# Performance work log

Hardware: AMD Instinct MI355X
Metric: run time of the kernel (lower is better)

Reference implementation:

```python
import jax, jax.numpy as jnp
import numpy as np

KERNELS = ("gaussian", "laplacian", "gaussian", "laplacian")
N, M, D, N_PER = 384, 384, 64, 200


def setup_inputs():
    key = jax.random.key(0)
    kx, ky, kb, kp = jax.random.split(key, 4)
    X = jax.random.normal(kx, (N, D), dtype=jnp.float32)
    Y = jax.random.normal(ky, (M, D), dtype=jnp.float32)
    # positive bandwidths of realistic magnitude for d=64 gaussian/laplacian kernels
    bandwidths = jax.random.uniform(kb, (4,), dtype=jnp.float32) * 8.0 + 4.0
    # each row is a random permutation of n+m indices (torch.randperm equivalent)
    perms = jax.vmap(lambda k: jax.random.permutation(k, N + M))(
        jax.random.split(kp, N_PER)).astype(jnp.int32)
    return {"X": X, "Y": Y, "bandwidths": bandwidths, "perms": perms}


def _pairwise_dist(Z):
    # torch.cdist(Z, Z, p=2); eps keeps sqrt grad finite on the zero diagonal
    sq = jnp.sum(Z * Z, axis=1)
    d2 = jnp.maximum(sq[:, None] + sq[None, :] - 2.0 * (Z @ Z.T), 0.0)
    return jnp.sqrt(d2 + 1e-12)


def reference(X, Y, bandwidths, perms):
    n, m = X.shape[0], Y.shape[0]
    Z = jnp.concatenate([X, Y], axis=0)            # [n+m, d]
    dist = _pairwise_dist(Z)                        # [n+m, n+m]
    idx = jnp.arange(min(n, m))
    perm_X, perm_Y = perms[:, :n], perms[:, n:]    # [n_per, n], [n_per, m]
    U, U_b = [], []
    for i, kern in enumerate(KERNELS):
        b = bandwidths[i]
        if kern == "gaussian":
            K = jnp.exp(-(dist * dist) / (b * b))
        else:  # laplacian
            K = jnp.exp(-dist / b)
        # mmd_u's in-place K_XY[diag]=0 mutates the view of K, so zero first
        K = K.at[idx, n + idx].set(0.0)
        K_XX, K_YY, K_XY = K[:n, :n], K[n:, n:], K[:n, n:]
        mmd = ((K_XX.sum() - jnp.trace(K_XX)) / (n * (n - 1))
               + (K_YY.sum() - jnp.trace(K_YY)) / (m * (m - 1))
               - 2.0 * K_XY.sum() / (n * m))
        U.append(mmd)
        # fast_perm: gather permuted blocks, zero diagonals, reduce per permutation
        diagK = jnp.diagonal(K)
        sXX = K[perm_X[:, :, None], perm_X[:, None, :]].sum((1, 2)) - diagK[perm_X].sum(1)
        sYY = K[perm_Y[:, :, None], perm_Y[:, None, :]].sum((1, 2)) - diagK[perm_Y].sum(1)
        sXY = (K[perm_X[:, :, None], perm_Y[:, None, :]].sum((1, 2))
               - K[perm_X[:, idx], perm_Y[:, idx]].sum(1))
        U_b.append(sXX / (n * (n - 1)) + sYY / (m * (m - 1)) - 2.0 * sXY / (n * m))
    U = jnp.stack(U)[:, None]    # [n_b, 1]  == compute_U_stats U.unsqueeze(1)
    U_b = jnp.stack(U_b)         # [n_b, n_per]
    return jnp.concatenate([U, U_b], axis=1)  # [n_b, 1 + n_per]
```

## Files before the change

### kernel.cpp

```cpp
#include <hip/hip_runtime.h>

#define NTOT 768
#define NHALF 384
#define DDIM 64
#define NPER 200
#define PPAD 256
#define NKER 4
#define CHUNK 192
#define NMB 12
#define NKH 2
#define NB_GEMM 384
#define NPART (NMB * NKH)

typedef __attribute__((ext_vector_type(8))) short short8;
typedef __attribute__((ext_vector_type(4))) float floatx4;

constexpr int K0SZ  = NTOT * NTOT;
constexpr int OF_KH = 0;
constexpr int KH_FLOATS = NKER * K0SZ / 2;
constexpr int OF_RS0 = OF_KH + KH_FLOATS;
constexpr int OF_RSX = OF_RS0 + NKER * NTOT;
constexpr int OF_RSY = OF_RSX + NKER * NTOT;
constexpr int OF_C   = OF_RSY + NKER * NTOT;
constexpr int OF_ROWM = OF_C + NKER * NHALF;
constexpr int OF_COLM = OF_ROWM + NKER * NTOT;
constexpr int OF_SCAL = OF_COLM + NKER * NTOT;
constexpr int OF_STT  = OF_SCAL + 16;
constexpr int STT_FLOATS = PPAD * NTOT / 2;
constexpr int OF_Q0P  = OF_STT + STT_FLOATS;

constexpr int SMEMF = CHUNK * 65 + DDIM + 32;

__device__ __forceinline__ unsigned short f2bf(float f) {
    unsigned int u = __float_as_uint(f);
    return (unsigned short)((u + 0x7FFFu + ((u >> 16) & 1u)) >> 16);
}
__device__ __forceinline__ float bf2f(unsigned short h) {
    return __uint_as_float(((unsigned int)h) << 16);
}

__global__ __launch_bounds__(256) void k_s1(const float* __restrict__ X,
                                            const float* __restrict__ Y,
                                            const float* __restrict__ bw,
                                            const int* __restrict__ perms,
                                            float* __restrict__ ws) {
    __shared__ float smem[SMEMF];
    float* zb   = smem;
    float* zaS  = smem + CHUNK * 65;
    float* redw = zaS + DDIM;
    int bid = blockIdx.x, tid = threadIdx.x;
    int wave = tid >> 6, lane = tid & 63;
    unsigned short* STT = (unsigned short*)(ws + OF_STT);
    unsigned short* KH  = (unsigned short*)(ws + OF_KH);

    if (bid < NPER) {
        if (tid < 192) {
            ((uint2*)(STT + bid * NTOT))[tid] = make_uint2(0u, 0u);
            if (bid < PPAD - NPER)
                ((uint2*)(STT + (NPER + bid) * NTOT))[tid] = make_uint2(0u, 0u);
        }
        __syncthreads();
        int v = perms[bid * NTOT + tid];
        STT[bid * NTOT + v] = 0x3F80;
        if (tid < NHALF - 256) {
            int v2 = perms[bid * NTOT + 256 + tid];
            STT[bid * NTOT + v2] = 0x3F80;
        }
        return;
    }

    int a = bid - NPER;
    const float* za = (a < NHALF) ? X + a * DDIM : Y + (a - NHALF) * DDIM;
    if (tid < DDIM) zaS[tid] = za[tid];
    float ib2[NKER], ib1[NKER];
#pragma unroll
    for (int k = 0; k < NKER; ++k) { float b = bw[k]; ib2[k] = 1.f / (b * b); ib1[k] = 1.f / b; }
    __syncthreads();
    float sqa = 0.f;
#pragma unroll
    for (int d = 0; d < DDIM; ++d) sqa = fmaf(zaS[d], zaS[d], sqa);
    float accX[NKER] = {0.f, 0.f, 0.f, 0.f};
    float accY[NKER] = {0.f, 0.f, 0.f, 0.f};

    for (int c0 = 0; c0 < NTOT; c0 += CHUNK) {
        __syncthreads();
        for (int idx = tid; idx < CHUNK * DDIM; idx += 256) {
            int r = idx >> 6, d = idx & 63;
            int gr = c0 + r;
            const float* zr = (gr < NHALF) ? X + gr * DDIM : Y + (gr - NHALF) * DDIM;
            zb[r * 65 + d] = zr[d];
        }
        __syncthreads();
        if (tid < CHUNK) {
            int b = c0 + tid;
            float dot = 0.f, sqb = 0.f;
#pragma unroll
            for (int d = 0; d < DDIM; ++d) {
                float zv = zb[tid * 65 + d];
                dot = fmaf(zaS[d], zv, dot);
                sqb = fmaf(zv, zv, sqb);
            }
            float d2 = (sqa + sqb) - 2.f * dot;
            if (b == a) d2 = 0.f;
            d2 = fmaxf(d2, 0.f);
            float d2e = d2 + 1e-12f;
            float dist = sqrtf(d2e);
#pragma unroll
            for (int k = 0; k < NKER; ++k) {
                float val = ((k & 1) == 0) ? __expf(-d2e * ib2[k]) : __expf(-dist * ib1[k]);
                KH[k * K0SZ + a * NTOT + b] = f2bf(val);
                if (b < NHALF) accX[k] += val; else accY[k] += val;
                if (a < NHALF && b == a + NHALF) ws[OF_C + k * NHALF + a] = val;
            }
        }
    }
    float vals[8];
#pragma unroll
    for (int k = 0; k < NKER; ++k) { vals[k] = accX[k]; vals[4 + k] = accY[k]; }
#pragma unroll
    for (int off = 32; off > 0; off >>= 1)
#pragma unroll
        for (int v = 0; v < 8; ++v) vals[v] += __shfl_down(vals[v], off, 64);
    __syncthreads();
    if (lane == 0)
#pragma unroll
        for (int v = 0; v < 8; ++v) redw[wave * 8 + v] = vals[v];
    __syncthreads();
    if (tid == 0) {
#pragma unroll
        for (int k = 0; k < NKER; ++k) {
            float sx = redw[k] + redw[8 + k] + redw[16 + k] + redw[24 + k];
            float sy = redw[4 + k] + redw[12 + k] + redw[20 + k] + redw[28 + k];
            ws[OF_RS0 + k * NTOT + a] = sx + sy;
            ws[OF_RSX + k * NTOT + a] = sx;
            ws[OF_RSY + k * NTOT + a] = sy;
        }
    }
}

__global__ __launch_bounds__(256) void k_s2(const float* __restrict__ bw,
                                            float* __restrict__ ws, float* __restrict__ out) {
    __shared__ float smem[256];
    int bid = blockIdx.x, tid = threadIdx.x;
    int wave = tid >> 6, lane = tid & 63;

    if (bid < NB_GEMM) {
        int mb = bid % NMB;
        int t  = bid / NMB;
        int nc = t & 3;
        int t2 = t >> 2;
        int k  = t2 & 3;
        int kh = t2 >> 2;
        int m0 = mb * 64 + wave * 16;
        int n0 = nc * 64;
        int row = lane & 15, quad = lane >> 4;
        const unsigned short* KH  = (const unsigned short*)(ws + OF_KH);
        const unsigned short* STT = (const unsigned short*)(ws + OF_STT);
        const unsigned short* aptr = KH + k * K0SZ + (m0 + row) * NTOT + quad * 8;
        floatx4 acc[4][2];
#pragma unroll
        for (int j = 0; j < 4; ++j)
#pragma unroll
            for (int h = 0; h < 2; ++h) acc[j][h] = (floatx4){0.f, 0.f, 0.f, 0.f};
        int kk0 = kh * (NTOT / 2);
        for (int kk = kk0; kk < kk0 + NTOT / 2; kk += 64) {
            short8 a0 = *(const short8*)(aptr + kk);
            short8 a1 = *(const short8*)(aptr + kk + 32);
#pragma unroll
            for (int j = 0; j < 4; ++j) {
                const unsigned short* bp = STT + (n0 + j * 16 + row) * NTOT + quad * 8 + kk;
                short8 b0 = *(const short8*)(bp);
                short8 b1 = *(const short8*)(bp + 32);
                acc[j][0] = __builtin_amdgcn_mfma_f32_16x16x32_bf16(a0, b0, acc[j][0], 0, 0, 0);
                acc[j][1] = __builtin_amdgcn_mfma_f32_16x16x32_bf16(a1, b1, acc[j][1], 0, 0, 0);
            }
        }
        __syncthreads();
#pragma unroll
        for (int j = 0; j < 4; ++j) {
            const unsigned short* sp = STT + (n0 + j * 16 + row) * NTOT + m0 + quad * 4;
            float p = 0.f;
#pragma unroll
            for (int r = 0; r < 4; ++r) p += (acc[j][0][r] + acc[j][1][r]) * bf2f(sp[r]);
            p += __shfl_down(p, 32, 64);
            p += __shfl_down(p, 16, 64);
            if (lane < 16) smem[wave * 64 + j * 16 + lane] = p;
        }
        __syncthreads();
        if (tid < 64) {
            float s = smem[tid] + smem[64 + tid] + smem[128 + tid] + smem[192 + tid];
            ws[OF_Q0P + (k * NPART + kh * NMB + mb) * PPAD + n0 + tid] = s;
        }
        return;
    }

    int k = bid - NB_GEMM;
    float v[5] = {0.f, 0.f, 0.f, 0.f, 0.f};
    for (int a = tid; a < NTOT; a += 256) v[0] += ws[OF_RS0 + k * NTOT + a];
    for (int a = tid; a < NHALF; a += 256) {
        v[1] += ws[OF_C + k * NHALF + a];
        v[2] += ws[OF_RSX + k * NTOT + a];
        v[3] += ws[OF_RSY + k * NTOT + NHALF + a];
        v[4] += ws[OF_RSY + k * NTOT + a];
    }
#pragma unroll
    for (int off = 32; off > 0; off >>= 1)
#pragma unroll
        for (int j = 0; j < 5; ++j) v[j] += __shfl_down(v[j], off, 64);
    __syncthreads();
    if (lane == 0)
#pragma unroll
        for (int j = 0; j < 5; ++j) smem[wave * 8 + j] = v[j];
    __syncthreads();
    if (tid == 0) {
        float tot0 = smem[0] + smem[8] + smem[16] + smem[24];
        float csum = smem[1] + smem[9] + smem[17] + smem[25];
        float sxx  = smem[2] + smem[10] + smem[18] + smem[26];
        float syy  = smem[3] + smem[11] + smem[19] + smem[27];
        float sxy  = smem[4] + smem[12] + smem[20] + smem[28];
        float b = bw[k];
        float dist0 = sqrtf(1e-12f);
        float dk = ((k & 1) == 0) ? expf(-(dist0 * dist0) / (b * b)) : expf(-dist0 / b);
        ws[OF_SCAL + k * 4 + 0] = tot0 - csum;
        ws[OF_SCAL + k * 4 + 1] = dk;
        double U = ((double)sxx - 384.0 * (double)dk) * (1.0 / 147072.0)
                 + ((double)syy - 384.0 * (double)dk) * (1.0 / 147072.0)
                 - 2.0 * ((double)sxy - (double)csum) * (1.0 / 147456.0);
        out[k * 201] = (float)U;
    }
    for (int idx = tid; idx < NTOT; idx += 256) {
        float r0 = ws[OF_RS0 + k * NTOT + idx];
        float cx = (idx < NHALF)  ? ws[OF_C + k * NHALF + idx] : 0.f;
        float cy = (idx >= NHALF) ? ws[OF_C + k * NHALF + idx - NHALF] : 0.f;
        ws[OF_ROWM + k * NTOT + idx] = r0 - cx;
        ws[OF_COLM + k * NTOT + idx] = r0 - cy;
    }
}

__global__ __launch_bounds__(256) void k_s3(const int* __restrict__ perms,
                                            const float* __restrict__ ws,
                                            float* __restrict__ out) {
    __shared__ float smem[128];
    int p = blockIdx.x, tid = threadIdx.x;
    int wave = tid >> 6, lane = tid & 63;
    const unsigned short* STT = (const unsigned short*)(ws + OF_STT);
    const unsigned short* KH  = (const unsigned short*)(ws + OF_KH);
    float v[16] = {0.f};
    for (int i = tid; i < NHALF; i += 256) {
        int a  = perms[p * NTOT + i];
        int bY = perms[p * NTOT + NHALF + i];
        float si  = bf2f(STT[p * NTOT + i]);
        float si2 = bf2f(STT[p * NTOT + NHALF + i]);
#pragma unroll
        for (int k = 0; k < NKER; ++k) {
            v[k * 4 + 0] += ws[OF_ROWM + k * NTOT + a];
            v[k * 4 + 1] += ws[OF_COLM + k * NTOT + a];
            float kv = bf2f(KH[k * K0SZ + a * NTOT + bY]);
            if (a < NHALF && bY == a + NHALF) kv = 0.f;
            v[k * 4 + 2] += kv;
            v[k * 4 + 3] += ws[OF_C + k * NHALF + i] * si * si2;
        }
    }
#pragma unroll
    for (int off = 32; off > 0; off >>= 1)
#pragma unroll
        for (int j = 0; j < 16; ++j) v[j] += __shfl_down(v[j], off, 64);
    __syncthreads();
    if (lane == 0)
#pragma unroll
        for (int j = 0; j < 16; ++j) smem[wave * 16 + j] = v[j];
    __syncthreads();
    if (tid < 16) smem[64 + tid] = smem[tid] + smem[16 + tid] + smem[32 + tid] + smem[48 + tid];
    __syncthreads();
    if (tid < NKER) {
        int k = tid;
        double rs = smem[64 + k * 4 + 0], cs = smem[64 + k * 4 + 1];
        double pair = smem[64 + k * 4 + 2], qc = smem[64 + k * 4 + 3];
        double total_mod = (double)ws[OF_SCAL + k * 4 + 0];
        double dk        = (double)ws[OF_SCAL + k * 4 + 1];
        double q = -qc;
#pragma unroll
        for (int j = 0; j < NPART; ++j) q += (double)ws[OF_Q0P + (k * NPART + j) * PPAD + p];
        double sXX = q - 384.0 * dk;
        double sYY = total_mod - rs - cs + q - 384.0 * dk;
        double sXY = rs - q - pair;
        out[k * 201 + 1 + p] =
            (float)(sXX * (1.0 / 147072.0) + sYY * (1.0 / 147072.0) - 2.0 * sXY * (1.0 / 147456.0));
    }
}

extern "C" void kernel_launch(void* const* d_in, const int* in_sizes, int n_in,
                              void* d_out, int out_size, void* d_ws, size_t ws_size,
                              hipStream_t stream) {
    const float* X     = (const float*)d_in[0];
    const float* Y     = (const float*)d_in[1];
    const float* bw    = (const float*)d_in[2];
    const int*   perms = (const int*)d_in[3];
    float* ws  = (float*)d_ws;
    float* out = (float*)d_out;

    k_s1<<<NPER + NTOT, 256, 0, stream>>>(X, Y, bw, perms, ws);
    k_s2<<<NB_GEMM + NKER, 256, 0, stream>>>(bw, ws, out);
    k_s3<<<NPER, 256, 0, stream>>>(perms, ws, out);
}
```

Baseline: 107.7 us.

## Tile pairwise-distance stage into 64x64 register-blocked tiles with partial row sums

The distance and kernel-matrix stage now uses 64x64 output tiles, with 4x4 register blocking per thread, instead of one block per row. Each tile writes per-tile partial row sums, and the reduction kernel combines them and also computes the row and column masks in the same pass. The aim is to cut redundant global and LDS reads of Z, use vectorized bf16 stores, and raise arithmetic reuse. The cost is a larger partial-sum buffer and an extra 12-way reduction in stage 2.

```diff
diff --git a/kernel.cpp b/kernel.cpp
--- a/kernel.cpp
+++ b/kernel.cpp
@@ -6,11 +6,12 @@
 #define NPER 200
 #define PPAD 256
 #define NKER 4
-#define CHUNK 192
 #define NMB 12
 #define NKH 2
 #define NB_GEMM 384
 #define NPART (NMB * NKH)
+#define NTILE 12
+#define LDSROW 68
 
 typedef __attribute__((ext_vector_type(8))) short short8;
 typedef __attribute__((ext_vector_type(4))) float floatx4;
@@ -18,10 +19,8 @@
 constexpr int K0SZ  = NTOT * NTOT;
 constexpr int OF_KH = 0;
 constexpr int KH_FLOATS = NKER * K0SZ / 2;
-constexpr int OF_RS0 = OF_KH + KH_FLOATS;
-constexpr int OF_RSX = OF_RS0 + NKER * NTOT;
-constexpr int OF_RSY = OF_RSX + NKER * NTOT;
-constexpr int OF_C   = OF_RSY + NKER * NTOT;
+constexpr int OF_P   = OF_KH + KH_FLOATS;
+constexpr int OF_C   = OF_P + NKER * NTILE * NTOT;
 constexpr int OF_ROWM = OF_C + NKER * NHALF;
 constexpr int OF_COLM = OF_ROWM + NKER * NTOT;
 constexpr int OF_SCAL = OF_COLM + NKER * NTOT;
@@ -29,8 +28,6 @@
 constexpr int STT_FLOATS = PPAD * NTOT / 2;
 constexpr int OF_Q0P  = OF_STT + STT_FLOATS;
 
-constexpr int SMEMF = CHUNK * 65 + DDIM + 32;
-
 __device__ __forceinline__ unsigned short f2bf(float f) {
     unsigned int u = __float_as_uint(f);
     return (unsigned short)((u + 0x7FFFu + ((u >> 16) & 1u)) >> 16);
@@ -44,12 +41,10 @@
                                             const float* __restrict__ bw,
                                             const int* __restrict__ perms,
                                             float* __restrict__ ws) {
-    __shared__ float smem[SMEMF];
-    float* zb   = smem;
-    float* zaS  = smem + CHUNK * 65;
-    float* redw = zaS + DDIM;
+    __shared__ float smem[128 * LDSROW + 128];
+    float* zb  = smem;
+    float* nrm = smem + 128 * LDSROW;
     int bid = blockIdx.x, tid = threadIdx.x;
-    int wave = tid >> 6, lane = tid & 63;
     unsigned short* STT = (unsigned short*)(ws + OF_STT);
     unsigned short* KH  = (unsigned short*)(ws + OF_KH);
 
@@ -69,38 +64,73 @@
         return;
     }
 
-    int a = bid - NPER;
-    const float* za = (a < NHALF) ? X + a * DDIM : Y + (a - NHALF) * DDIM;
-    if (tid < DDIM) zaS[tid] = za[tid];
+    int t  = bid - NPER;
+    int at = t / NTILE, bt = t % NTILE;
+    int a0 = at * 64, b0 = bt * 64;
+    int ta = tid >> 4, tb = tid & 15;
+
     float ib2[NKER], ib1[NKER];
 #pragma unroll
     for (int k = 0; k < NKER; ++k) { float b = bw[k]; ib2[k] = 1.f / (b * b); ib1[k] = 1.f / b; }
-    __syncthreads();
-    float sqa = 0.f;
-#pragma unroll
-    for (int d = 0; d < DDIM; ++d) sqa = fmaf(zaS[d], zaS[d], sqa);
-    float accX[NKER] = {0.f, 0.f, 0.f, 0.f};
-    float accY[NKER] = {0.f, 0.f, 0.f, 0.f};
-
-    for (int c0 = 0; c0 < NTOT; c0 += CHUNK) {
-        __syncthreads();
-        for (int idx = tid; idx < CHUNK * DDIM; idx += 256) {
-            int r = idx >> 6, d = idx & 63;
-            int gr = c0 + r;
-            const float* zr = (gr < NHALF) ? X + gr * DDIM : Y + (gr - NHALF) * DDIM;
-            zb[r * 65 + d] = zr[d];
-        }
-        __syncthreads();
-        if (tid < CHUNK) {
-            int b = c0 + tid;
-            float dot = 0.f, sqb = 0.f;
-#pragma unroll
-            for (int d = 0; d < DDIM; ++d) {
-                float zv = zb[tid * 65 + d];
-                dot = fmaf(zaS[d], zv, dot);
-                sqb = fmaf(zv, zv, sqb);
+
+#pragma unroll
+    for (int it = 0; it < 8; ++it) {
+        int idx = it * 256 + tid;
+        int j = idx >> 4, qf = idx & 15;
+        int g = (j < 64) ? a0 + j : b0 + (j - 64);
+        const float* zr = (g < NHALF) ? X + g * DDIM : Y + (g - NHALF) * DDIM;
+        *(float4*)(zb + j * LDSROW + qf * 4) = *(const float4*)(zr + qf * 4);
+    }
+    __syncthreads();
+    if (tid < 128) {
+        float s = 0.f;
+        const float* zr = zb + tid * LDSROW;
+#pragma unroll
+        for (int d = 0; d < DDIM; d += 4) {
+            float4 zv = *(const float4*)(zr + d);
+            s += zv.x * zv.x + zv.y * zv.y + zv.z * zv.z + zv.w * zv.w;
+        }
+        nrm[tid] = s;
+    }
+    __syncthreads();
+
+    float acc[4][4];
+#pragma unroll
+    for (int r = 0; r < 4; ++r)
+#pragma unroll
+        for (int c = 0; c < 4; ++c) acc[r][c] = 0.f;
+#pragma unroll
+    for (int s = 0; s < 16; ++s) {
+        float4 av[4], bv[4];
+#pragma unroll
+        for (int r = 0; r < 4; ++r) av[r] = *(const float4*)(zb + (ta * 4 + r) * LDSROW + s * 4);
+#pragma unroll
+        for (int c = 0; c < 4; ++c) bv[c] = *(const float4*)(zb + (64 + tb * 4 + c) * LDSROW + s * 4);
+#pragma unroll
+        for (int r = 0; r < 4; ++r)
+#pragma unroll
+            for (int c = 0; c < 4; ++c) {
+                acc[r][c] = fmaf(av[r].x, bv[c].x, acc[r][c]);
+                acc[r][c] = fmaf(av[r].y, bv[c].y, acc[r][c]);
+                acc[r][c] = fmaf(av[r].z, bv[c].z, acc[r][c]);
+                acc[r][c] = fmaf(av[r].w, bv[c].w, acc[r][c]);
             }
-            float d2 = (sqa + sqb) - 2.f * dot;
+    }
+
+    float rs[4][NKER];
+#pragma unroll
+    for (int r = 0; r < 4; ++r)
+#pragma unroll
+        for (int k = 0; k < NKER; ++k) rs[r][k] = 0.f;
+
+#pragma unroll
+    for (int r = 0; r < 4; ++r) {
+        int a = a0 + ta * 4 + r;
+        ushort4 us[NKER];
+#pragma unroll
+        for (int c = 0; c < 4; ++c) {
+            int b = b0 + tb * 4 + c;
+            float d2 = (nrm[ta * 4 + r] + nrm[64 + tb * 4 + c]) - 2.f * acc[r][c];
             if (b == a) d2 = 0.f;
             d2 = fmaxf(d2, 0.f);
             float d2e = d2 + 1e-12f;
@@ -108,32 +138,30 @@
 #pragma unroll
             for (int k = 0; k < NKER; ++k) {
                 float val = ((k & 1) == 0) ? __expf(-d2e * ib2[k]) : __expf(-dist * ib1[k]);
-                KH[k * K0SZ + a * NTOT + b] = f2bf(val);
-                if (b < NHALF) accX[k] += val; else accY[k] += val;
-                if (a < NHALF && b == a + NHALF) ws[OF_C + k * NHALF + a] = val;
+                rs[r][k] += val;
+                unsigned short h = f2bf(val);
+                if (c == 0) us[k].x = h; else if (c == 1) us[k].y = h;
+                else if (c == 2) us[k].z = h; else us[k].w = h;
+                if (bt == at + 6 && tb == ta && c == r)
+                    ws[OF_C + k * NHALF + a] = val;
             }
         }
-    }
-    float vals[8];
-#pragma unroll
-    for (int k = 0; k < NKER; ++k) { vals[k] = accX[k]; vals[4 + k] = accY[k]; }
-#pragma unroll
-    for (int off = 32; off > 0; off >>= 1)
-#pragma unroll
-        for (int v = 0; v < 8; ++v) vals[v] += __shfl_down(vals[v], off, 64);
-    __syncthreads();
-    if (lane == 0)
-#pragma unroll
-        for (int v = 0; v < 8; ++v) redw[wave * 8 + v] = vals[v];
-    __syncthreads();
-    if (tid == 0) {
+#pragma unroll
+        for (int k = 0; k < NKER; ++k)
+            *(ushort4*)(KH + k * K0SZ + a * NTOT + b0 + tb * 4) = us[k];
+    }
+
+#pragma unroll
+    for (int off = 8; off > 0; off >>= 1)
+#pragma unroll
+        for (int r = 0; r < 4; ++r)
+#pragma unroll
+            for (int k = 0; k < NKER; ++k) rs[r][k] += __shfl_down(rs[r][k], off, 64);
+    if (tb == 0) {
 #pragma unroll
         for (int k = 0; k < NKER; ++k) {
-            float sx = redw[k] + redw[8 + k] + redw[16 + k] + redw[24 + k];
-            float sy = redw[4 + k] + redw[12 + k] + redw[20 + k] + redw[28 + k];
-            ws[OF_RS0 + k * NTOT + a] = sx + sy;
-            ws[OF_RSX + k * NTOT + a] = sx;
-            ws[OF_RSY + k * NTOT + a] = sy;
+            float4 pv = make_float4(rs[0][k], rs[1][k], rs[2][k], rs[3][k]);
+            *(float4*)(ws + OF_P + (k * NTILE + bt) * NTOT + a0 + ta * 4) = pv;
         }
     }
 }
@@ -195,13 +223,22 @@
     }
 
     int k = bid - NB_GEMM;
+    const float* Pk = ws + OF_P + k * (NTILE * NTOT);
     float v[5] = {0.f, 0.f, 0.f, 0.f, 0.f};
-    for (int a = tid; a < NTOT; a += 256) v[0] += ws[OF_RS0 + k * NTOT + a];
-    for (int a = tid; a < NHALF; a += 256) {
-        v[1] += ws[OF_C + k * NHALF + a];
-        v[2] += ws[OF_RSX + k * NTOT + a];
-        v[3] += ws[OF_RSY + k * NTOT + NHALF + a];
-        v[4] += ws[OF_RSY + k * NTOT + a];
+    for (int a = tid; a < NTOT; a += 256) {
+        float rsx = 0.f, rsy = 0.f;
+#pragma unroll
+        for (int j = 0; j < 6; ++j)  rsx += Pk[j * NTOT + a];
+#pragma unroll
+        for (int j = 6; j < 12; ++j) rsy += Pk[j * NTOT + a];
+        float rs0 = rsx + rsy;
+        float cx = (a < NHALF)  ? ws[OF_C + k * NHALF + a] : 0.f;
+        float cy = (a >= NHALF) ? ws[OF_C + k * NHALF + a - NHALF] : 0.f;
+        ws[OF_ROWM + k * NTOT + a] = rs0 - cx;
+        ws[OF_COLM + k * NTOT + a] = rs0 - cy;
+        v[0] += rs0;
+        if (a < NHALF) { v[1] += cx; v[2] += rsx; v[4] += rsy; }
+        else           { v[3] += rsy; }
     }
 #pragma unroll
     for (int off = 32; off > 0; off >>= 1)
@@ -228,13 +265,6 @@
                  - 2.0 * ((double)sxy - (double)csum) * (1.0 / 147456.0);
         out[k * 201] = (float)U;
     }
-    for (int idx = tid; idx < NTOT; idx += 256) {
-        float r0 = ws[OF_RS0 + k * NTOT + idx];
-        float cx = (idx < NHALF)  ? ws[OF_C + k * NHALF + idx] : 0.f;
-        float cy = (idx >= NHALF) ? ws[OF_C + k * NHALF + idx - NHALF] : 0.f;
-        ws[OF_ROWM + k * NTOT + idx] = r0 - cx;
-        ws[OF_COLM + k * NTOT + idx] = r0 - cy;
-    }
 }
 
 __global__ __launch_bounds__(256) void k_s3(const int* __restrict__ perms,
@@ -299,7 +329,7 @@
     float* ws  = (float*)d_ws;
     float* out = (float*)d_out;
 
-    k_s1<<<NPER + NTOT, 256, 0, stream>>>(X, Y, bw, perms, ws);
+    k_s1<<<NPER + NTILE * NTILE, 256, 0, stream>>>(X, Y, bw, perms, ws);
     k_s2<<<NB_GEMM + NKER, 256, 0, stream>>>(bw, ws, out);
     k_s3<<<NPER, 256, 0, stream>>>(perms, ws, out);
 }
```

New measurement: 105.0 us. 2.4% less time.
